# Kernel tuning notes

Measured on AMD Instinct MI355X. Metric: run time of the kernel, lower is better.

## Reference

```python
import jax, jax.numpy as jnp
import numpy as np

B, C, D, H, W = 4, 128, 16, 16, 16
P = 64  # proj_dim (spatial branch is dead code in the original fusion; params omitted)


def setup_inputs() -> dict:
    key = jax.random.key(0)
    ks = jax.random.split(key, 10)
    lin = lambda k, o, i: 0.02 * jax.random.normal(k, (o, i), jnp.float32)
    return {
        "x": jax.random.normal(ks[0], (B, C, D, H, W), jnp.float32),
        "ln_g": jnp.ones((C,), jnp.float32),
        "ln_b": jnp.zeros((C,), jnp.float32),
        "Wq": lin(ks[1], C, C), "bq": jnp.zeros((C,), jnp.float32),
        "Wk": lin(ks[2], C, C), "bk": jnp.zeros((C,), jnp.float32),
        "Wvc": lin(ks[3], C, C), "bvc": jnp.zeros((C,), jnp.float32),
        "Wvch": lin(ks[4], C, C), "bvch": jnp.zeros((C,), jnp.float32),
        "Wconv": 0.02 * jax.random.normal(ks[5], (2, C, 3, 3, 3), jnp.float32),
        "bconv": jnp.zeros((2,), jnp.float32),
        "Wg": lin(ks[6], 3, C), "bg": jnp.zeros((3,), jnp.float32),
    }


def reference(x, ln_g, ln_b, Wq, bq, Wk, bk, Wvc, bvc, Wvch, bvch, Wconv, bconv, Wg, bg):
    b, c, d, h, w = x.shape
    n = d * h * w
    # LayerNorm over channels (permute to channels-last)
    xp = jnp.transpose(x, (0, 2, 3, 4, 1))                      # (B,D,H,W,C)
    mu = jnp.mean(xp, axis=-1, keepdims=True)
    var = jnp.mean((xp - mu) ** 2, axis=-1, keepdims=True)
    xn = (xp - mu) * jax.lax.rsqrt(var + 1e-5) * ln_g + ln_b     # (B,D,H,W,C)
    x_norm = jnp.transpose(xn, (0, 4, 1, 2, 3))                  # (B,C,D,H,W)
    # Causal Growth Field prediction: Conv3d C->2, k=3, SAME padding
    cgf = jax.lax.conv_general_dilated(
        x_norm, Wconv, (1, 1, 1), "SAME",
        dimension_numbers=("NCDHW", "OIDHW", "NCDHW")) + bconv[None, :, None, None, None]
    # Token sequence (B,N,C); same flattening order as x_norm.view(B,C,-1).transpose(1,2)
    xf = xn.reshape(b, n, c)
    q = jnp.einsum("bnc,oc->bno", xf, Wq) + bq
    k = jnp.einsum("bnc,oc->bno", xf, Wk) + bk
    # --- causal branch: full NxN attention ---
    vc = jnp.einsum("bnc,oc->bno", xf, Wvc) + bvc
    attn_causal = jax.nn.softmax(jnp.einsum("bnc,bmc->bnm", q, k) / (c ** 0.5), axis=-1)
    out_causal = jnp.einsum("bnm,bmc->bnc", attn_causal, vc)
    # --- channel branch: CxC attention ---
    vch = jnp.einsum("bnc,oc->bno", xf, Wvch) + bvch
    attn_channel = jax.nn.softmax(jnp.einsum("bnc,bnd->bcd", q, k) / (n ** 0.5), axis=-1)
    out_channel = jnp.einsum("bcd,bnd->bnc", attn_channel, vch)
    # --- gated fusion (original uses only weights 0 and 2; spatial branch is dead code) ---
    pooled = jnp.mean(x, axis=(2, 3, 4))                          # (B,C)
    weights = jax.nn.softmax(pooled @ Wg.T + bg, axis=-1)         # (B,3)
    fused = (weights[:, 0][:, None, None] * out_causal
             + weights[:, 2][:, None, None] * out_channel)        # (B,N,C)
    output = x + jnp.transpose(fused, (0, 2, 1)).reshape(b, c, d, h, w)
    return (output, cgf)
```

## Files before the change

kernel.cpp:

```cpp
#include <hip/hip_runtime.h>
#include <math.h>

#define CH   128
#define NSP  4096
#define BATCH 4
#define BIG  (BATCH*NSP*CH)
#define KCHUNKS 64
#define FKSPLIT 4
#define MB (1024*1024)

typedef short short8 __attribute__((ext_vector_type(8)));
typedef float floatx4 __attribute__((ext_vector_type(4)));

__device__ __forceinline__ unsigned short f2bu(float f) {
  union { float f; unsigned u; } v; v.f = f;
  unsigned r = v.u + 0x7fffu + ((v.u >> 16) & 1u);
  return (unsigned short)(r >> 16);
}
__device__ __forceinline__ float b2f(unsigned short h) {
  union { unsigned u; float f; } v; v.u = ((unsigned)h) << 16;
  return v.f;
}

__global__ __launch_bounds__(256) void ln_kernel(const float* __restrict__ x,
    const float* __restrict__ g, const float* __restrict__ bta,
    unsigned short* __restrict__ xfb) {
  __shared__ float tile[128][65];
  __shared__ float pS[4][64];
  __shared__ float pQ[4][64];
  __shared__ float mu_s[64], rs_s[64];
  int t = threadIdx.x;
  int b  = blockIdx.x >> 6;
  int n0 = (blockIdx.x & 63) << 6;
  for (int i = t; i < 8192; i += 256) {
    int c = i >> 6, n = i & 63;
    tile[c][n] = x[(size_t)(b*CH + c)*NSP + n0 + n];
  }
  __syncthreads();
  {
    int n = t & 63, part = t >> 6;
    float s = 0.f, qq = 0.f;
    for (int c = part; c < 128; c += 4) { float v = tile[c][n]; s += v; qq += v*v; }
    pS[part][n] = s; pQ[part][n] = qq;
  }
  __syncthreads();
  if (t < 64) {
    float s = pS[0][t] + pS[1][t] + pS[2][t] + pS[3][t];
    float qq = pQ[0][t] + pQ[1][t] + pQ[2][t] + pQ[3][t];
    float mu = s * (1.f/128.f);
    float var = qq * (1.f/128.f) - mu*mu;
    mu_s[t] = mu;
    rs_s[t] = rsqrtf(var + 1e-5f);
  }
  __syncthreads();
  for (int i = t; i < 8192; i += 256) {
    int n = i >> 7, c = i & 127;
    float v = (tile[c][n] - mu_s[n]) * rs_s[n] * g[c] + bta[c];
    xfb[(size_t)(b*NSP + n0 + n)*CH + c] = f2bu(v);
  }
}

__global__ __launch_bounds__(256) void pooled_kernel(const float* __restrict__ x,
                                                     float* __restrict__ pooled) {
  int bc = blockIdx.x; int t = threadIdx.x;
  const float4* p = (const float4*)(x + (size_t)bc*NSP);
  float s = 0.f;
  for (int i = t; i < 1024; i += 256) { float4 v = p[i]; s += v.x+v.y+v.z+v.w; }
  for (int off = 32; off; off >>= 1) s += __shfl_xor(s, off, 64);
  __shared__ float red[4];
  if ((t & 63) == 0) red[t >> 6] = s;
  __syncthreads();
  if (t == 0) pooled[bc] = (red[0]+red[1]+red[2]+red[3]) * (1.f/4096.f);
}

__global__ void gate_kernel(const float* __restrict__ pooled, const float* __restrict__ Wg,
                            const float* __restrict__ bg, float* __restrict__ wgt) {
  __shared__ float lg[4][3];
  int t = threadIdx.x;
  if (t < 12) {
    int b = t / 3, j = t % 3;
    float s = bg[j];
    const float* pr = pooled + b*CH;
    const float* wr = Wg + j*CH;
    for (int c = 0; c < CH; ++c) s += pr[c]*wr[c];
    lg[b][j] = s;
  }
  __syncthreads();
  if (t < 4) {
    float a = lg[t][0], b2 = lg[t][1], c = lg[t][2];
    float m = fmaxf(a, fmaxf(b2, c));
    float e0 = __expf(a-m), e1 = __expf(b2-m), e2 = __expf(c-m);
    float inv = 1.f/(e0+e1+e2);
    wgt[t*3+0] = e0*inv; wgt[t*3+1] = e1*inv; wgt[t*3+2] = e2*inv;
  }
}

__global__ __launch_bounds__(256) void conv_kernel(const unsigned short* __restrict__ xfb,
    const float* __restrict__ Wc, const float* __restrict__ bc_, float* __restrict__ cgf) {
  __shared__ float Wl[27*256];
  int t = threadIdx.x;
  for (int i = t; i < 6912; i += 256) {
    int tap = i >> 8;
    int rem = i & 255;
    int o = rem >> 7, c = rem & 127;
    Wl[i] = Wc[o*3456 + c*27 + tap];
  }
  __syncthreads();
  int cg = t & 15, spl = t >> 4;
  int sp = blockIdx.x*16 + spl;
  int b = sp >> 12, n = sp & 4095;
  int z = n >> 8, y = (n >> 4) & 15, xw = n & 15;
  const unsigned short* xb = xfb + (size_t)b*NSP*CH + cg*8;
  float a0 = 0.f, a1 = 0.f;
  for (int kd = 0; kd < 3; ++kd) {
    int zz = z + kd - 1; if ((unsigned)zz >= 16u) continue;
    for (int kh = 0; kh < 3; ++kh) {
      int yy = y + kh - 1; if ((unsigned)yy >= 16u) continue;
      #pragma unroll
      for (int kw = 0; kw < 3; ++kw) {
        int xx = xw + kw - 1; if ((unsigned)xx >= 16u) continue;
        int nn = (zz << 8) + (yy << 4) + xx;
        short8 xv = *(const short8*)(xb + (size_t)nn*CH);
        int tap = (kd*3 + kh)*3 + kw;
        const float* wbase = &Wl[tap*256 + cg*8];
        float4 w00 = *(const float4*)(wbase);
        float4 w01 = *(const float4*)(wbase + 4);
        float4 w10 = *(const float4*)(wbase + 128);
        float4 w11 = *(const float4*)(wbase + 132);
        float x0 = b2f((unsigned short)xv[0]), x1 = b2f((unsigned short)xv[1]);
        float x2 = b2f((unsigned short)xv[2]), x3 = b2f((unsigned short)xv[3]);
        float x4 = b2f((unsigned short)xv[4]), x5 = b2f((unsigned short)xv[5]);
        float x6 = b2f((unsigned short)xv[6]), x7 = b2f((unsigned short)xv[7]);
        a0 += x0*w00.x + x1*w00.y + x2*w00.z + x3*w00.w
            + x4*w01.x + x5*w01.y + x6*w01.z + x7*w01.w;
        a1 += x0*w10.x + x1*w10.y + x2*w10.z + x3*w10.w
            + x4*w11.x + x5*w11.y + x6*w11.z + x7*w11.w;
      }
    }
  }
  #pragma unroll
  for (int off = 1; off <= 8; off <<= 1) {
    a0 += __shfl_xor(a0, off, 64);
    a1 += __shfl_xor(a1, off, 64);
  }
  if (cg == 0) {
    cgf[b*8192 + n]        = a0 + bc_[0];
    cgf[b*8192 + 4096 + n] = a1 + bc_[1];
  }
}

__global__ __launch_bounds__(256) void wcast_kernel(const float* __restrict__ Wq,
    const float* __restrict__ Wk, const float* __restrict__ Wvc,
    const float* __restrict__ Wvch, unsigned short* __restrict__ Wb) {
  int idx = blockIdx.x*256 + threadIdx.x;
  int pj = idx >> 14, wi = idx & 16383;
  const float* src = (pj == 0) ? Wq : (pj == 1) ? Wk : (pj == 2) ? Wvc : Wvch;
  Wb[idx] = f2bu(src[wi]);
}

__global__ __launch_bounds__(256) void proj_mfma_kernel(
    const unsigned short* __restrict__ xfb, const unsigned short* __restrict__ Wb,
    const float* __restrict__ bq, const float* __restrict__ bk,
    const float* __restrict__ bvc, const float* __restrict__ bvch,
    unsigned short* __restrict__ q, unsigned short* __restrict__ k,
    unsigned short* __restrict__ vc, unsigned short* __restrict__ vch) {
  __shared__ __align__(16) unsigned short Ws[128][136];
  int t = threadIdx.x;
  int lane = t & 63, w = t >> 6;
  int id = lane & 15, quad = lane >> 4;
  int pj = blockIdx.y;
  int r0 = blockIdx.x*128 + w*32;

  const unsigned short* Wp = Wb + ((size_t)pj << 14);
  for (int i = t; i < 2048; i += 256) {
    int rr = i >> 4, c8 = (i & 15) << 3;
    *(short8*)&Ws[rr][c8] = *(const short8*)(Wp + rr*CH + c8);
  }
  short8 af[2][4];
  #pragma unroll
  for (int m = 0; m < 2; ++m)
    #pragma unroll
    for (int kc = 0; kc < 4; ++kc)
      af[m][kc] = *(const short8*)(xfb + (size_t)(r0 + m*16 + id)*CH + kc*32 + quad*8);
  __syncthreads();

  floatx4 acc[2][8];
  #pragma unroll
  for (int m = 0; m < 2; ++m)
    #pragma unroll
    for (int nt = 0; nt < 8; ++nt) acc[m][nt] = (floatx4){0.f,0.f,0.f,0.f};
  #pragma unroll
  for (int nt = 0; nt < 8; ++nt)
    #pragma unroll
    for (int kc = 0; kc < 4; ++kc) {
      short8 bf = *(const short8*)&Ws[nt*16 + id][kc*32 + quad*8];
      acc[0][nt] = __builtin_amdgcn_mfma_f32_16x16x32_bf16(af[0][kc], bf, acc[0][nt], 0, 0, 0);
      acc[1][nt] = __builtin_amdgcn_mfma_f32_16x16x32_bf16(af[1][kc], bf, acc[1][nt], 0, 0, 0);
    }

  const float* bias = (pj == 0) ? bq : (pj == 1) ? bk : (pj == 2) ? bvc : bvch;
  unsigned short* Y = (pj == 0) ? q : (pj == 1) ? k : (pj == 2) ? vc : vch;
  #pragma unroll
  for (int nt = 0; nt < 8; ++nt) {
    float bsv = bias[nt*16 + id];
    #pragma unroll
    for (int m = 0; m < 2; ++m)
      #pragma unroll
      for (int r = 0; r < 4; ++r) {
        int row = r0 + m*16 + quad*4 + r;
        Y[(size_t)row*CH + nt*16 + id] = f2bu(acc[m][nt][r] + bsv);
      }
  }
}

__global__ __launch_bounds__(256) void vtrans_kernel(const unsigned short* __restrict__ vc,
                                                     unsigned short* __restrict__ vct) {
  __shared__ unsigned short T[128][72];
  int t = threadIdx.x;
  int b = blockIdx.x >> 6, n0 = (blockIdx.x & 63) << 6;
  for (int i = t; i < 1024; i += 256) {
    int n = i >> 4, c0 = (i & 15) << 3;
    short8 v = *(const short8*)&vc[(size_t)(b*NSP + n0 + n)*CH + c0];
    #pragma unroll
    for (int j = 0; j < 8; ++j) T[c0+j][n] = (unsigned short)v[j];
  }
  __syncthreads();
  for (int i = t; i < 1024; i += 256) {
    int c = i >> 3, k8 = (i & 7) << 3;
    *(short8*)&vct[((size_t)b*CH + c)*NSP + n0 + k8] = *(short8*)&T[c][k8];
  }
}

__global__ __launch_bounds__(256) void chscore_kernel(const unsigned short* __restrict__ q,
    const unsigned short* __restrict__ k, float* __restrict__ Sp) {
  __shared__ unsigned short Qt[128][72];
  __shared__ unsigned short Kt[128][72];
  int t = threadIdx.x;
  int lane = t & 63, w = t >> 6;
  int id = lane & 15, quad = lane >> 4;
  int p = blockIdx.x;
  int b = blockIdx.y;
  const unsigned short* qb = q + (size_t)b*NSP*CH;
  const unsigned short* kb = k + (size_t)b*NSP*CH;
  int nbase = p*64;

  #pragma unroll
  for (int it = 0; it < 4; ++it) {
    int task = t + it*256;
    int c = task & 127, r0 = (task >> 7) << 3;
    short8 vq, vk;
    #pragma unroll
    for (int j = 0; j < 8; ++j) {
      size_t off = (size_t)(nbase + r0 + j)*CH + c;
      vq[j] = (short)qb[off];
      vk[j] = (short)kb[off];
    }
    *(short8*)&Qt[c][r0] = vq;
    *(short8*)&Kt[c][r0] = vk;
  }
  __syncthreads();

  floatx4 acc[2][8];
  #pragma unroll
  for (int mt = 0; mt < 2; ++mt)
    #pragma unroll
    for (int nt = 0; nt < 8; ++nt) acc[mt][nt] = (floatx4){0.f,0.f,0.f,0.f};
  #pragma unroll
  for (int kc = 0; kc < 2; ++kc) {
    short8 af0 = *(const short8*)&Qt[w*32 + id     ][kc*32 + quad*8];
    short8 af1 = *(const short8*)&Qt[w*32 + 16 + id][kc*32 + quad*8];
    #pragma unroll
    for (int nt = 0; nt < 8; ++nt) {
      short8 bf = *(const short8*)&Kt[nt*16 + id][kc*32 + quad*8];
      acc[0][nt] = __builtin_amdgcn_mfma_f32_16x16x32_bf16(af0, bf, acc[0][nt], 0, 0, 0);
      acc[1][nt] = __builtin_amdgcn_mfma_f32_16x16x32_bf16(af1, bf, acc[1][nt], 0, 0, 0);
    }
  }
  float* outp = Sp + ((size_t)(p*BATCH + b) << 14);
  #pragma unroll
  for (int mt = 0; mt < 2; ++mt)
    #pragma unroll
    for (int nt = 0; nt < 8; ++nt)
      #pragma unroll
      for (int r = 0; r < 4; ++r) {
        int c = w*32 + mt*16 + quad*4 + r;
        int d = nt*16 + id;
        outp[c*CH + d] = acc[mt][nt][r];
      }
}

__global__ __launch_bounds__(64) void chsoftmax_kernel(const float* __restrict__ Sp,
                                                       unsigned short* __restrict__ Sb) {
  int row = blockIdx.x;
  int b = row >> 7, c = row & 127;
  int t = threadIdx.x;
  float s0 = 0.f, s1 = 0.f;
  #pragma unroll 4
  for (int p = 0; p < KCHUNKS; ++p) {
    const float* r = Sp + (((size_t)(p*BATCH + b) << 7) + c)*CH;
    s0 += r[t]; s1 += r[t+64];
  }
  const float sc = 1.f/64.f;
  s0 *= sc; s1 *= sc;
  float m = fmaxf(s0, s1);
  for (int off = 32; off; off >>= 1) m = fmaxf(m, __shfl_xor(m, off, 64));
  float p0 = __expf(s0 - m), p1 = __expf(s1 - m);
  float s = p0 + p1;
  for (int off = 32; off; off >>= 1) s += __shfl_xor(s, off, 64);
  float inv = 1.f/s;
  unsigned short* r = Sb + (size_t)row*CH;
  r[t]    = f2bu(p0*inv);
  r[t+64] = f2bu(p1*inv);
}

__global__ __launch_bounds__(256) void chout_mfma_kernel(
    const unsigned short* __restrict__ vchb, const unsigned short* __restrict__ Sb,
    float* __restrict__ och) {
  __shared__ __align__(16) unsigned short As[128][136];
  int t = threadIdx.x;
  int lane = t & 63, w = t >> 6;
  int id = lane & 15, quad = lane >> 4;
  int b = blockIdx.x >> 5;
  int r0 = blockIdx.x*128 + w*32;

  const unsigned short* Sp = Sb + ((size_t)b << 14);
  for (int i = t; i < 2048; i += 256) {
    int rr = i >> 4, c8 = (i & 15) << 3;
    *(short8*)&As[rr][c8] = *(const short8*)(Sp + rr*CH + c8);
  }
  short8 af[2][4];
  #pragma unroll
  for (int m = 0; m < 2; ++m)
    #pragma unroll
    for (int kc = 0; kc < 4; ++kc)
      af[m][kc] = *(const short8*)(vchb + (size_t)(r0 + m*16 + id)*CH + kc*32 + quad*8);
  __syncthreads();

  floatx4 acc[2][8];
  #pragma unroll
  for (int m = 0; m < 2; ++m)
    #pragma unroll
    for (int nt = 0; nt < 8; ++nt) acc[m][nt] = (floatx4){0.f,0.f,0.f,0.f};
  #pragma unroll
  for (int nt = 0; nt < 8; ++nt)
    #pragma unroll
    for (int kc = 0; kc < 4; ++kc) {
      short8 bf = *(const short8*)&As[nt*16 + id][kc*32 + quad*8];
      acc[0][nt] = __builtin_amdgcn_mfma_f32_16x16x32_bf16(af[0][kc], bf, acc[0][nt], 0, 0, 0);
      acc[1][nt] = __builtin_amdgcn_mfma_f32_16x16x32_bf16(af[1][kc], bf, acc[1][nt], 0, 0, 0);
    }
  #pragma unroll
  for (int nt = 0; nt < 8; ++nt)
    #pragma unroll
    for (int m = 0; m < 2; ++m)
      #pragma unroll
      for (int r = 0; r < 4; ++r) {
        int row = r0 + m*16 + quad*4 + r;
        och[(size_t)row*CH + nt*16 + id] = acc[m][nt][r];
      }
}

__global__ __launch_bounds__(256) void flash_part_kernel(
    const unsigned short* __restrict__ Qg, const unsigned short* __restrict__ Kg,
    const unsigned short* __restrict__ Vtg,
    unsigned short* __restrict__ Opart, float* __restrict__ lpart) {
  __shared__ __align__(16) unsigned short Ks[64][136];
  __shared__ __align__(16) unsigned short Vt[128][72];
  __shared__ __align__(16) unsigned short Ps[4][32][68];
  int t = threadIdx.x;
  int lane = t & 63, w = t >> 6;
  int id = lane & 15, quad = lane >> 4;
  int blk = blockIdx.x;
  int x = blk & 7, y = blk >> 3;
  int tile = y & 31;
  int b = x >> 1;
  int ks = (x & 1) + ((y >> 5) << 1);
  int n0 = tile << 7;
  int r0 = n0 + w*32;

  const unsigned short* Qb = Qg  + (size_t)b*NSP*CH;
  const unsigned short* Kb = Kg  + (size_t)b*NSP*CH;
  const unsigned short* Vb = Vtg + (size_t)b*CH*NSP;

  int kr[4], kc8[4], vr[4], vn[4];
  #pragma unroll
  for (int it = 0; it < 4; ++it) {
    int task = t + it*256;
    kr[it] = task >> 4; kc8[it] = (task & 15) << 3;
    vr[it] = task >> 3; vn[it]  = (task & 7) << 3;
  }

  short8 qf[2][4];
  #pragma unroll
  for (int m = 0; m < 2; ++m)
    #pragma unroll
    for (int kc = 0; kc < 4; ++kc)
      qf[m][kc] = *(const short8*)(Qb + (size_t)(r0 + m*16 + id)*CH + kc*32 + quad*8);

  floatx4 O[2][8];
  #pragma unroll
  for (int m = 0; m < 2; ++m)
    #pragma unroll
    for (int ct = 0; ct < 8; ++ct) O[m][ct] = (floatx4){0.f,0.f,0.f,0.f};
  float lrun[2][4];
  #pragma unroll
  for (int m = 0; m < 2; ++m)
    #pragma unroll
    for (int r = 0; r < 4; ++r) lrun[m][r] = 0.f;

  const float scale = 0.08838834764831845f;

  short8 kreg[4], vreg[4];
  {
    int kbase = ks*1024;
    #pragma unroll
    for (int it = 0; it < 4; ++it) {
      kreg[it] = *(const short8*)(Kb + (size_t)(kbase + kr[it])*CH + kc8[it]);
      vreg[it] = *(const short8*)(Vb + (size_t)vr[it]*NSP + kbase + vn[it]);
    }
  }

  for (int kt = 0; kt < 16; ++kt) {
    __syncthreads();
    #pragma unroll
    for (int it = 0; it < 4; ++it) {
      *(short8*)&Ks[kr[it]][kc8[it]] = kreg[it];
      *(short8*)&Vt[vr[it]][vn[it]]  = vreg[it];
    }
    __syncthreads();
    if (kt < 15) {
      int kbase = ks*1024 + (kt+1)*64;
      #pragma unroll
      for (int it = 0; it < 4; ++it) {
        kreg[it] = *(const short8*)(Kb + (size_t)(kbase + kr[it])*CH + kc8[it]);
        vreg[it] = *(const short8*)(Vb + (size_t)vr[it]*NSP + kbase + vn[it]);
      }
    }

    floatx4 S[2][4];
    #pragma unroll
    for (int nt = 0; nt < 4; ++nt) {
      floatx4 a0 = (floatx4){0.f,0.f,0.f,0.f};
      floatx4 a1 = (floatx4){0.f,0.f,0.f,0.f};
      #pragma unroll
      for (int kc = 0; kc < 4; ++kc) {
        short8 kf = *(const short8*)&Ks[nt*16 + id][kc*32 + quad*8];
        a0 = __builtin_amdgcn_mfma_f32_16x16x32_bf16(qf[0][kc], kf, a0, 0, 0, 0);
        a1 = __builtin_amdgcn_mfma_f32_16x16x32_bf16(qf[1][kc], kf, a1, 0, 0, 0);
      }
      S[0][nt] = a0; S[1][nt] = a1;
    }
    #pragma unroll
    for (int m = 0; m < 2; ++m) {
      float rs[4] = {0.f,0.f,0.f,0.f};
      #pragma unroll
      for (int nt = 0; nt < 4; ++nt)
        #pragma unroll
        for (int r = 0; r < 4; ++r) {
          float p = __expf(S[m][nt][r] * scale);
          rs[r] += p;
          Ps[w][m*16 + quad*4 + r][nt*16 + id] = f2bu(p);
        }
      #pragma unroll
      for (int off = 1; off <= 8; off <<= 1)
        #pragma unroll
        for (int r = 0; r < 4; ++r) rs[r] += __shfl_xor(rs[r], off, 64);
      #pragma unroll
      for (int r = 0; r < 4; ++r) lrun[m][r] += rs[r];
    }
    #pragma unroll
    for (int nc = 0; nc < 2; ++nc) {
      short8 pf0 = *(const short8*)&Ps[w][id     ][nc*32 + quad*8];
      short8 pf1 = *(const short8*)&Ps[w][16 + id][nc*32 + quad*8];
      #pragma unroll
      for (int ct = 0; ct < 8; ++ct) {
        short8 vf = *(const short8*)&Vt[ct*16 + id][nc*32 + quad*8];
        O[0][ct] = __builtin_amdgcn_mfma_f32_16x16x32_bf16(pf0, vf, O[0][ct], 0, 0, 0);
        O[1][ct] = __builtin_amdgcn_mfma_f32_16x16x32_bf16(pf1, vf, O[1][ct], 0, 0, 0);
      }
    }
  }

  unsigned short* Op = Opart + (size_t)ks*BIG + (size_t)b*NSP*CH;
  #pragma unroll
  for (int m = 0; m < 2; ++m)
    #pragma unroll
    for (int ct = 0; ct < 8; ++ct)
      #pragma unroll
      for (int r = 0; r < 4; ++r) {
        int row = r0 + m*16 + quad*4 + r;
        Op[(size_t)row*CH + ct*16 + id] = f2bu(O[m][ct][r]);
      }
  if (id == 0) {
    float* lp = lpart + (size_t)ks*BATCH*NSP + (size_t)b*NSP;
    #pragma unroll
    for (int m = 0; m < 2; ++m)
      #pragma unroll
      for (int r = 0; r < 4; ++r)
        lp[r0 + m*16 + quad*4 + r] = lrun[m][r];
  }
}

__global__ __launch_bounds__(256) void fuse_kernel(const float* __restrict__ x,
    const unsigned short* __restrict__ Opart, const float* __restrict__ lpart,
    const float* __restrict__ och, const float* __restrict__ wgt,
    float* __restrict__ out) {
  __shared__ float T[128][65];
  __shared__ float linv[64];
  int t = threadIdx.x;
  int b  = blockIdx.x >> 6;
  int n0 = (blockIdx.x & 63) << 6;
  float w0 = wgt[b*3 + 0], w2 = wgt[b*3 + 2];
  if (t < 64) {
    float l = 0.f;
    #pragma unroll
    for (int p = 0; p < FKSPLIT; ++p)
      l += lpart[(size_t)p*BATCH*NSP + b*NSP + n0 + t];
    linv[t] = 1.f / l;
  }
  __syncthreads();
  const float* ochb = och + (size_t)(b*NSP + n0)*CH;
  for (int i = t; i < 8192; i += 256) {
    int n = i >> 7, c = i & 127;
    size_t oidx = (size_t)(b*NSP + n0 + n)*CH + c;
    float o = 0.f;
    #pragma unroll
    for (int p = 0; p < FKSPLIT; ++p) o += b2f(Opart[(size_t)p*BIG + oidx]);
    T[c][n] = w0*o*linv[n] + w2*ochb[(size_t)n*CH + c];
  }
  __syncthreads();
  for (int i = t; i < 8192; i += 256) {
    int c = i >> 6, n = i & 63;
    size_t idx = (size_t)(b*CH + c)*NSP + n0 + n;
    out[idx] = x[idx] + T[c][n];
  }
}

extern "C" void kernel_launch(void* const* d_in, const int* in_sizes, int n_in,
                              void* d_out, int out_size, void* d_ws, size_t ws_size,
                              hipStream_t stream) {
  (void)in_sizes; (void)n_in; (void)out_size; (void)ws_size;
  const float* x     = (const float*)d_in[0];
  const float* ln_g  = (const float*)d_in[1];
  const float* ln_b  = (const float*)d_in[2];
  const float* Wq    = (const float*)d_in[3];
  const float* bq    = (const float*)d_in[4];
  const float* Wk    = (const float*)d_in[5];
  const float* bk    = (const float*)d_in[6];
  const float* Wvc   = (const float*)d_in[7];
  const float* bvc   = (const float*)d_in[8];
  const float* Wvch  = (const float*)d_in[9];
  const float* bvch  = (const float*)d_in[10];
  const float* Wconv = (const float*)d_in[11];
  const float* bconv = (const float*)d_in[12];
  const float* Wg    = (const float*)d_in[13];
  const float* bg    = (const float*)d_in[14];

  float* out = (float*)d_out;
  float* cgf = out + (size_t)BIG;

  char* base = (char*)d_ws;
  float* och  = (float*)(base);
  unsigned short* Opart = (unsigned short*)(base + 8*(size_t)MB);
  float* Sp             = (float*)(base + 8*(size_t)MB);
  unsigned short* vcb   = (unsigned short*)(base + 24*(size_t)MB);
  float* lpart  = (float*)(base + 32*(size_t)MB);
  unsigned short* Schb = (unsigned short*)(base + 32*(size_t)MB + 512*1024);
  float* pooled = (float*)(base + 32*(size_t)MB + 768*1024);
  float* wgt    = pooled + BATCH*CH;
  unsigned short* qb   = (unsigned short*)(base + 33*(size_t)MB);
  unsigned short* kb   = (unsigned short*)(base + 37*(size_t)MB);
  unsigned short* vct  = (unsigned short*)(base + 41*(size_t)MB);
  unsigned short* vchb = (unsigned short*)(base + 45*(size_t)MB);
  unsigned short* Wb   = (unsigned short*)(base + 49*(size_t)MB);
  unsigned short* xfb  = (unsigned short*)(base + 49*(size_t)MB + 256*1024);

  ln_kernel     <<<256, 256, 0, stream>>>(x, ln_g, ln_b, xfb);
  pooled_kernel <<<512, 256, 0, stream>>>(x, pooled);
  gate_kernel   <<<1,   64,  0, stream>>>(pooled, Wg, bg, wgt);
  wcast_kernel  <<<256, 256, 0, stream>>>(Wq, Wk, Wvc, Wvch, Wb);
  conv_kernel   <<<1024, 256, 0, stream>>>(xfb, Wconv, bconv, cgf);
  proj_mfma_kernel<<<dim3(128,4), 256, 0, stream>>>(xfb, Wb, bq, bk, bvc, bvch,
                                                    qb, kb, vcb, vchb);
  vtrans_kernel <<<256, 256, 0, stream>>>(vcb, vct);
  chscore_kernel<<<dim3(KCHUNKS, BATCH), 256, 0, stream>>>(qb, kb, Sp);
  chsoftmax_kernel<<<512, 64, 0, stream>>>(Sp, Schb);
  chout_mfma_kernel<<<128, 256, 0, stream>>>(vchb, Schb, och);
  flash_part_kernel<<<512, 256, 0, stream>>>(qb, kb, vct, Opart, lpart);
  fuse_kernel   <<<256, 256, 0, stream>>>(x, Opart, lpart, och, wgt, out);
}
```

Measured before the change: 222.4 us.

## Fuse gate and weight-cast kernels, fold q scale, MFMA row sums

Removes the separate gate and weight-cast kernels: weights are converted to bf16 inside the projection kernel and the gate softmax is computed in each fuse block. The attention scale is folded into q at projection time, with the channel softmax compensated. Flash row sums are computed via MFMA against a ones vector instead of shuffle reductions. This trades launch overhead and VALU work for redundant weight conversion per block and slightly different rounding.

```diff
diff --git a/kernel.cpp b/kernel.cpp
--- a/kernel.cpp
+++ b/kernel.cpp
@@ -11,6 +11,8 @@
 
 typedef short short8 __attribute__((ext_vector_type(8)));
 typedef float floatx4 __attribute__((ext_vector_type(4)));
+
+#define QSCALE 0.08838834764831845f
 
 __device__ __forceinline__ unsigned short f2bu(float f) {
   union { float f; unsigned u; } v; v.f = f;
@@ -71,28 +73,6 @@
   if ((t & 63) == 0) red[t >> 6] = s;
   __syncthreads();
   if (t == 0) pooled[bc] = (red[0]+red[1]+red[2]+red[3]) * (1.f/4096.f);
-}
-
-__global__ void gate_kernel(const float* __restrict__ pooled, const float* __restrict__ Wg,
-                            const float* __restrict__ bg, float* __restrict__ wgt) {
-  __shared__ float lg[4][3];
-  int t = threadIdx.x;
-  if (t < 12) {
-    int b = t / 3, j = t % 3;
-    float s = bg[j];
-    const float* pr = pooled + b*CH;
-    const float* wr = Wg + j*CH;
-    for (int c = 0; c < CH; ++c) s += pr[c]*wr[c];
-    lg[b][j] = s;
-  }
-  __syncthreads();
-  if (t < 4) {
-    float a = lg[t][0], b2 = lg[t][1], c = lg[t][2];
-    float m = fmaxf(a, fmaxf(b2, c));
-    float e0 = __expf(a-m), e1 = __expf(b2-m), e2 = __expf(c-m);
-    float inv = 1.f/(e0+e1+e2);
-    wgt[t*3+0] = e0*inv; wgt[t*3+1] = e1*inv; wgt[t*3+2] = e2*inv;
-  }
 }
 
 __global__ __launch_bounds__(256) void conv_kernel(const unsigned short* __restrict__ xfb,
@@ -149,17 +129,10 @@
   }
 }
 
-__global__ __launch_bounds__(256) void wcast_kernel(const float* __restrict__ Wq,
-    const float* __restrict__ Wk, const float* __restrict__ Wvc,
-    const float* __restrict__ Wvch, unsigned short* __restrict__ Wb) {
-  int idx = blockIdx.x*256 + threadIdx.x;
-  int pj = idx >> 14, wi = idx & 16383;
-  const float* src = (pj == 0) ? Wq : (pj == 1) ? Wk : (pj == 2) ? Wvc : Wvch;
-  Wb[idx] = f2bu(src[wi]);
-}
-
 __global__ __launch_bounds__(256) void proj_mfma_kernel(
-    const unsigned short* __restrict__ xfb, const unsigned short* __restrict__ Wb,
+    const unsigned short* __restrict__ xfb,
+    const float* __restrict__ Wq, const float* __restrict__ Wk,
+    const float* __restrict__ Wvc, const float* __restrict__ Wvch,
     const float* __restrict__ bq, const float* __restrict__ bk,
     const float* __restrict__ bvc, const float* __restrict__ bvch,
     unsigned short* __restrict__ q, unsigned short* __restrict__ k,
@@ -171,10 +144,14 @@
   int pj = blockIdx.y;
   int r0 = blockIdx.x*128 + w*32;
 
-  const unsigned short* Wp = Wb + ((size_t)pj << 14);
+  const float* Wp = (pj == 0) ? Wq : (pj == 1) ? Wk : (pj == 2) ? Wvc : Wvch;
   for (int i = t; i < 2048; i += 256) {
     int rr = i >> 4, c8 = (i & 15) << 3;
-    *(short8*)&Ws[rr][c8] = *(const short8*)(Wp + rr*CH + c8);
+    const float* src = Wp + rr*CH + c8;
+    short8 pk;
+    #pragma unroll
+    for (int j = 0; j < 8; ++j) pk[j] = (short)f2bu(src[j]);
+    *(short8*)&Ws[rr][c8] = pk;
   }
   short8 af[2][4];
   #pragma unroll
@@ -200,6 +177,7 @@
 
   const float* bias = (pj == 0) ? bq : (pj == 1) ? bk : (pj == 2) ? bvc : bvch;
   unsigned short* Y = (pj == 0) ? q : (pj == 1) ? k : (pj == 2) ? vc : vch;
+  float osc = (pj == 0) ? QSCALE : 1.f;
   #pragma unroll
   for (int nt = 0; nt < 8; ++nt) {
     float bsv = bias[nt*16 + id];
@@ -208,7 +186,7 @@
       #pragma unroll
       for (int r = 0; r < 4; ++r) {
         int row = r0 + m*16 + quad*4 + r;
-        Y[(size_t)row*CH + nt*16 + id] = f2bu(acc[m][nt][r] + bsv);
+        Y[(size_t)row*CH + nt*16 + id] = f2bu((acc[m][nt][r] + bsv) * osc);
       }
   }
 }
@@ -300,7 +278,7 @@
     const float* r = Sp + (((size_t)(p*BATCH + b) << 7) + c)*CH;
     s0 += r[t]; s1 += r[t+64];
   }
-  const float sc = 1.f/64.f;
+  const float sc = (1.f/64.f) / QSCALE;
   s0 *= sc; s1 *= sc;
   float m = fmaxf(s0, s1);
   for (int off = 32; off; off >>= 1) m = fmaxf(m, __shfl_xor(m, off, 64));
@@ -402,13 +380,11 @@
   for (int m = 0; m < 2; ++m)
     #pragma unroll
     for (int ct = 0; ct < 8; ++ct) O[m][ct] = (floatx4){0.f,0.f,0.f,0.f};
-  float lrun[2][4];
-  #pragma unroll
-  for (int m = 0; m < 2; ++m)
-    #pragma unroll
-    for (int r = 0; r < 4; ++r) lrun[m][r] = 0.f;
-
-  const float scale = 0.08838834764831845f;
+  floatx4 lacc0 = (floatx4){0.f,0.f,0.f,0.f};
+  floatx4 lacc1 = (floatx4){0.f,0.f,0.f,0.f};
+  short8 ones;
+  #pragma unroll
+  for (int j = 0; j < 8; ++j) ones[j] = (short)0x3F80;
 
   short8 kreg[4], vreg[4];
   {
@@ -451,27 +427,19 @@
       S[0][nt] = a0; S[1][nt] = a1;
     }
     #pragma unroll
-    for (int m = 0; m < 2; ++m) {
-      float rs[4] = {0.f,0.f,0.f,0.f};
+    for (int m = 0; m < 2; ++m)
       #pragma unroll
       for (int nt = 0; nt < 4; ++nt)
         #pragma unroll
-        for (int r = 0; r < 4; ++r) {
-          float p = __expf(S[m][nt][r] * scale);
-          rs[r] += p;
-          Ps[w][m*16 + quad*4 + r][nt*16 + id] = f2bu(p);
-        }
-      #pragma unroll
-      for (int off = 1; off <= 8; off <<= 1)
-        #pragma unroll
-        for (int r = 0; r < 4; ++r) rs[r] += __shfl_xor(rs[r], off, 64);
-      #pragma unroll
-      for (int r = 0; r < 4; ++r) lrun[m][r] += rs[r];
-    }
+        for (int r = 0; r < 4; ++r)
+          Ps[w][m*16 + quad*4 + r][nt*16 + id] = f2bu(__expf(S[m][nt][r]));
+
     #pragma unroll
     for (int nc = 0; nc < 2; ++nc) {
       short8 pf0 = *(const short8*)&Ps[w][id     ][nc*32 + quad*8];
       short8 pf1 = *(const short8*)&Ps[w][16 + id][nc*32 + quad*8];
+      lacc0 = __builtin_amdgcn_mfma_f32_16x16x32_bf16(pf0, ones, lacc0, 0, 0, 0);
+      lacc1 = __builtin_amdgcn_mfma_f32_16x16x32_bf16(pf1, ones, lacc1, 0, 0, 0);
       #pragma unroll
       for (int ct = 0; ct < 8; ++ct) {
         short8 vf = *(const short8*)&Vt[ct*16 + id][nc*32 + quad*8];
@@ -494,31 +462,51 @@
   if (id == 0) {
     float* lp = lpart + (size_t)ks*BATCH*NSP + (size_t)b*NSP;
     #pragma unroll
-    for (int m = 0; m < 2; ++m)
-      #pragma unroll
-      for (int r = 0; r < 4; ++r)
-        lp[r0 + m*16 + quad*4 + r] = lrun[m][r];
+    for (int r = 0; r < 4; ++r) {
+      lp[r0 + quad*4 + r]      = lacc0[r];
+      lp[r0 + 16 + quad*4 + r] = lacc1[r];
+    }
   }
 }
 
 __global__ __launch_bounds__(256) void fuse_kernel(const float* __restrict__ x,
     const unsigned short* __restrict__ Opart, const float* __restrict__ lpart,
-    const float* __restrict__ och, const float* __restrict__ wgt,
+    const float* __restrict__ och, const float* __restrict__ pooled,
+    const float* __restrict__ Wg, const float* __restrict__ bg,
     float* __restrict__ out) {
   __shared__ float T[128][65];
   __shared__ float linv[64];
+  __shared__ float wsh[2];
   int t = threadIdx.x;
   int b  = blockIdx.x >> 6;
   int n0 = (blockIdx.x & 63) << 6;
-  float w0 = wgt[b*3 + 0], w2 = wgt[b*3 + 2];
   if (t < 64) {
     float l = 0.f;
     #pragma unroll
     for (int p = 0; p < FKSPLIT; ++p)
       l += lpart[(size_t)p*BATCH*NSP + b*NSP + n0 + t];
     linv[t] = 1.f / l;
-  }
-  __syncthreads();
+    float p0 = pooled[b*CH + t], p1 = pooled[b*CH + 64 + t];
+    float d0 = p0*Wg[t]       + p1*Wg[64 + t];
+    float d1 = p0*Wg[128 + t] + p1*Wg[192 + t];
+    float d2 = p0*Wg[256 + t] + p1*Wg[320 + t];
+    #pragma unroll
+    for (int off = 32; off; off >>= 1) {
+      d0 += __shfl_xor(d0, off, 64);
+      d1 += __shfl_xor(d1, off, 64);
+      d2 += __shfl_xor(d2, off, 64);
+    }
+    if (t == 0) {
+      d0 += bg[0]; d1 += bg[1]; d2 += bg[2];
+      float m = fmaxf(d0, fmaxf(d1, d2));
+      float e0 = __expf(d0 - m), e1 = __expf(d1 - m), e2 = __expf(d2 - m);
+      float inv = 1.f/(e0 + e1 + e2);
+      wsh[0] = e0*inv;
+      wsh[1] = e2*inv;
+    }
+  }
+  __syncthreads();
+  float w0 = wsh[0], w2 = wsh[1];
   const float* ochb = och + (size_t)(b*NSP + n0)*CH;
   for (int i = t; i < 8192; i += 256) {
     int n = i >> 7, c = i & 127;
@@ -567,25 +555,22 @@
   float* lpart  = (float*)(base + 32*(size_t)MB);
   unsigned short* Schb = (unsigned short*)(base + 32*(size_t)MB + 512*1024);
   float* pooled = (float*)(base + 32*(size_t)MB + 768*1024);
-  float* wgt    = pooled + BATCH*CH;
   unsigned short* qb   = (unsigned short*)(base + 33*(size_t)MB);
   unsigned short* kb   = (unsigned short*)(base + 37*(size_t)MB);
   unsigned short* vct  = (unsigned short*)(base + 41*(size_t)MB);
   unsigned short* vchb = (unsigned short*)(base + 45*(size_t)MB);
-  unsigned short* Wb   = (unsigned short*)(base + 49*(size_t)MB);
-  unsigned short* xfb  = (unsigned short*)(base + 49*(size_t)MB + 256*1024);
+  unsigned short* xfb  = (unsigned short*)(base + 49*(size_t)MB);
 
   ln_kernel     <<<256, 256, 0, stream>>>(x, ln_g, ln_b, xfb);
   pooled_kernel <<<512, 256, 0, stream>>>(x, pooled);
-  gate_kernel   <<<1,   64,  0, stream>>>(pooled, Wg, bg, wgt);
-  wcast_kernel  <<<256, 256, 0, stream>>>(Wq, Wk, Wvc, Wvch, Wb);
   conv_kernel   <<<1024, 256, 0, stream>>>(xfb, Wconv, bconv, cgf);
-  proj_mfma_kernel<<<dim3(128,4), 256, 0, stream>>>(xfb, Wb, bq, bk, bvc, bvch,
+  proj_mfma_kernel<<<dim3(128,4), 256, 0, stream>>>(xfb, Wq, Wk, Wvc, Wvch,
+                                                    bq, bk, bvc, bvch,
                                                     qb, kb, vcb, vchb);
   vtrans_kernel <<<256, 256, 0, stream>>>(vcb, vct);
   chscore_kernel<<<dim3(KCHUNKS, BATCH), 256, 0, stream>>>(qb, kb, Sp);
   chsoftmax_kernel<<<512, 64, 0, stream>>>(Sp, Schb);
   chout_mfma_kernel<<<128, 256, 0, stream>>>(vchb, Schb, och);
   flash_part_kernel<<<512, 256, 0, stream>>>(qb, kb, vct, Opart, lpart);
-  fuse_kernel   <<<256, 256, 0, stream>>>(x, Opart, lpart, och, wgt, out);
-}
+  fuse_kernel   <<<256, 256, 0, stream>>>(x, Opart, lpart, och, pooled, Wg, bg, out);
+}
```

New measurement: 227.3 us. 1.02x slower.
